# Kernel optimization log

Measured on AMD Instinct MI355X. Metric: run time of the kernel, lower is better.

## Reference

```python
import jax, jax.numpy as jnp
import numpy as np

H, DI, N, R, B, L, K = 1024, 2048, 16, 64, 1, 2048, 4


def setup_inputs() -> dict:
    key = jax.random.key(0)
    ks = jax.random.split(key, 12)
    s = 0.02
    x = jax.random.normal(ks[0], (B, L, H), dtype=jnp.float32)
    in_proj_w = jax.random.normal(ks[1], (2 * DI, H), dtype=jnp.float32) * s
    in_proj_b = jax.random.normal(ks[2], (2 * DI,), dtype=jnp.float32) * s
    conv_w = jax.random.normal(ks[3], (DI, 1, K), dtype=jnp.float32) * s
    conv_b = jax.random.normal(ks[4], (DI,), dtype=jnp.float32) * s
    x_proj_w = jax.random.normal(ks[5], (R + 2 * N, DI), dtype=jnp.float32) * s
    dt_init_std = R ** (-0.5)
    dt_proj_w = jax.random.uniform(ks[6], (DI, R), dtype=jnp.float32, minval=-dt_init_std, maxval=dt_init_std)
    dt = jnp.exp(jax.random.uniform(ks[7], (DI,), dtype=jnp.float32) * (np.log(0.1) - np.log(0.001)) + np.log(0.001))
    dt = jnp.clip(dt, 0.0001, None)
    dt_proj_b = dt + jnp.log(-jnp.expm1(-dt))
    A_log = jnp.log(jnp.broadcast_to(jnp.arange(1, N + 1, dtype=jnp.float32)[None, :], (DI, N)))
    D = jnp.ones((DI,), dtype=jnp.float32)
    out_proj_w = jax.random.normal(ks[8], (H, DI), dtype=jnp.float32) * s
    return {"x": x, "in_proj_w": in_proj_w, "in_proj_b": in_proj_b, "conv_w": conv_w,
            "conv_b": conv_b, "x_proj_w": x_proj_w, "dt_proj_w": dt_proj_w,
            "dt_proj_b": dt_proj_b, "A_log": A_log, "D": D, "out_proj_w": out_proj_w}


def _mamba_fwd(x, in_proj_w, in_proj_b, conv_w, conv_b, x_proj_w, dt_proj_w, dt_proj_b, A_log, D, out_proj_w):
    b, l, _ = x.shape
    x_and_res = x @ in_proj_w.T + in_proj_b               # [b, l, 2*DI]
    xc, res = jnp.split(x_and_res, 2, axis=-1)
    # causal depthwise conv1d (padding K-1 then truncate to l == left-pad only)
    xt = jnp.transpose(xc, (0, 2, 1))                     # [b, DI, l]
    conv = jax.lax.conv_general_dilated(
        xt, conv_w, window_strides=(1,), padding=[(K - 1, 0)],
        dimension_numbers=("NCH", "OIH", "NCH"), feature_group_count=DI)
    conv = conv + conv_b[None, :, None]
    xs = jnp.transpose(jax.nn.silu(conv), (0, 2, 1))      # [b, l, DI]
    # SSM
    A = -jnp.exp(A_log.astype(jnp.float32))               # [DI, N]
    x_dbl = xs @ x_proj_w.T                               # [b, l, R+2N]
    delta, Bm, Cm = jnp.split(x_dbl, [R, R + N], axis=-1)
    delta = jax.nn.softplus(delta @ dt_proj_w.T + dt_proj_b)   # [b, l, DI]
    deltaA = jnp.exp(delta[..., None] * A[None, None])         # [b, l, DI, N]
    deltaB_u = delta[..., None] * Bm[:, :, None, :] * xs[..., None]

    def comb(c1, c2):
        a1, u1 = c1
        a2, u2 = c2
        return a2 * a1, a2 * u1 + u2

    _, h = jax.lax.associative_scan(comb, (deltaA, deltaB_u), axis=1)
    y = jnp.einsum("bldn,bln->bld", h, Cm) + xs * D.astype(jnp.float32)
    y = y * jax.nn.silu(res)
    return y @ out_proj_w.T                               # [b, l, H]


def reference(x, in_proj_w, in_proj_b, conv_w, conv_b, x_proj_w, dt_proj_w, dt_proj_b, A_log, D, out_proj_w):
    return _mamba_fwd(x, in_proj_w, in_proj_b, conv_w, conv_b, x_proj_w,
                      dt_proj_w, dt_proj_b, A_log, D, out_proj_w)
```

## Files before the change

kernel.cpp:

```cpp
#include <hip/hip_runtime.h>
#include <hip/hip_bf16.h>
#include <math.h>

#define H_DIM 1024
#define DI    2048
#define NS    16
#define RR    64
#define LL    2048
#define NC    32
#define CL    64
#define KSPL  16

typedef __bf16 bf16x8 __attribute__((ext_vector_type(8)));
typedef __bf16 bf16x4 __attribute__((ext_vector_type(4)));
typedef float  f32x4  __attribute__((ext_vector_type(4)));

__device__ __forceinline__ float silu_f(float x)  { return x / (1.f + __expf(-x)); }
__device__ __forceinline__ float softplus_f(float x) {
    const float l = __logf(1.f + __expf(x));
    return x > 15.f ? x : l;
}

__device__ __forceinline__ void gload16(const void* g, void* l) {
    __builtin_amdgcn_global_load_lds(
        (const __attribute__((address_space(1))) void*)g,
        (__attribute__((address_space(3))) void*)l, 16, 0, 0);
}

__device__ __forceinline__ void f2b4(const float* __restrict__ in,
                                     __bf16* __restrict__ out)
{
    float4 v = *(const float4*)in;
    bf16x4 o;
    o[0] = (__bf16)v.x; o[1] = (__bf16)v.y; o[2] = (__bf16)v.z; o[3] = (__bf16)v.w;
    *(bf16x4*)out = o;
}

#define SEG0 (LL * H_DIM)
#define SEG1 (2 * DI * H_DIM)
#define SEG2 (H_DIM * DI)
#define SEG3 (DI * RR)
#define SEG4 (128 * DI)
#define CUM0 SEG0
#define CUM1 (CUM0 + SEG1)
#define CUM2 (CUM1 + SEG2)
#define CUM3 (CUM2 + SEG3)
#define CUMT (CUM3 + SEG4)

__global__ __launch_bounds__(256) void convert_all_k(
    const float* __restrict__ x,    const float* __restrict__ in_w,
    const float* __restrict__ outw, const float* __restrict__ dtw,
    const float* __restrict__ xpw,
    __bf16* __restrict__ x_bf,    __bf16* __restrict__ inw_bf,
    __bf16* __restrict__ outw_bf, __bf16* __restrict__ dtw_bf,
    __bf16* __restrict__ xpw_pad)
{
    const int i = (blockIdx.x * 256 + threadIdx.x) * 4;
    if (i < CUM0) {
        f2b4(x + i, x_bf + i);
    } else if (i < CUM1) {
        const int o = i - CUM0;  f2b4(in_w + o, inw_bf + o);
    } else if (i < CUM2) {
        const int o = i - CUM1;  f2b4(outw + o, outw_bf + o);
    } else if (i < CUM3) {
        const int o = i - CUM2;  f2b4(dtw + o, dtw_bf + o);
    } else if (i < CUMT) {
        const int o = i - CUM3;
        const int row = o >> 11;
        if (row < 96) {
            f2b4(xpw + o, xpw_pad + o);
        } else {
            bf16x4 z; z[0] = z[1] = z[2] = z[3] = (__bf16)0.f;
            *(bf16x4*)&xpw_pad[o] = z;
        }
    }
}

__global__ __launch_bounds__(256) void reduce_xdbl_k(
    const float* __restrict__ part, float* __restrict__ xdbl,
    __bf16* __restrict__ xdbl_bf)
{
    const int idx = blockIdx.x * 256 + threadIdx.x;
    float s = 0.f;
    #pragma unroll
    for (int z = 0; z < KSPL; ++z) s += part[(size_t)z * (LL * 96) + idx];
    xdbl[idx] = s;
    xdbl_bf[idx] = (__bf16)s;
}

__global__ __launch_bounds__(256) void gemm_inproj_k(
    const __bf16* __restrict__ A,
    const __bf16* __restrict__ W,
    const float* __restrict__ bias,
    __bf16* __restrict__ xc_bf,
    __bf16* __restrict__ res_bf)
{
    __shared__ __bf16 smA[128 * 32];
    __shared__ __bf16 smB[128 * 32];
    const int t    = threadIdx.x;
    const int lane = t & 63;
    const int m0 = blockIdx.y * 128, n0 = blockIdx.x * 128;
    const int wr = ((t >> 6) >> 1) * 64;
    const int wc = ((t >> 6) & 1) * 64;

    const int srow = t >> 2;
    const int skof = (t & 3) * 8;
    const int lds_base = (t >> 6) * 512;

    const int offA = (wr + (lane & 15)) * 32 + ((lane >> 4) * 8);
    const int offB = (wc + (lane & 15)) * 32 + ((lane >> 4) * 8);

    f32x4 acc[4][4] = {};

    for (int k0 = 0; k0 < H_DIM; k0 += 32) {
        gload16(A + (size_t)(m0 + srow)      * H_DIM + k0 + skof, &smA[lds_base]);
        gload16(A + (size_t)(m0 + 64 + srow) * H_DIM + k0 + skof, &smA[2048 + lds_base]);
        gload16(W + (size_t)(n0 + srow)      * H_DIM + k0 + skof, &smB[lds_base]);
        gload16(W + (size_t)(n0 + 64 + srow) * H_DIM + k0 + skof, &smB[2048 + lds_base]);
        __syncthreads();

        bf16x8 af[4], bfr[4];
        #pragma unroll
        for (int m = 0; m < 4; ++m) af[m]  = *(const bf16x8*)&smA[offA + m * 512];
        #pragma unroll
        for (int n = 0; n < 4; ++n) bfr[n] = *(const bf16x8*)&smB[offB + n * 512];
        #pragma unroll
        for (int m = 0; m < 4; ++m)
            #pragma unroll
            for (int n = 0; n < 4; ++n)
                acc[m][n] = __builtin_amdgcn_mfma_f32_16x16x32_bf16(
                    af[m], bfr[n], acc[m][n], 0, 0, 0);
        __syncthreads();
    }

    __bf16* outp = (n0 < DI) ? xc_bf : res_bf;
    const int ncol0 = (n0 < DI) ? n0 : n0 - DI;
    const int rbase = m0 + wr + ((lane >> 4) << 2);
    const int cbase = ncol0 + wc + (lane & 15);
    #pragma unroll
    for (int n = 0; n < 4; ++n) {
        const int col = cbase + n * 16;
        const float bv = bias[(n0 < DI ? 0 : DI) + col];
        #pragma unroll
        for (int m = 0; m < 4; ++m)
            #pragma unroll
            for (int j = 0; j < 4; ++j)
                outp[(size_t)(rbase + m * 16 + j) * DI + col] =
                    (__bf16)(acc[m][n][j] + bv);
    }
}

template<int BIAS, int ACT, int SPLITK>
__global__ __launch_bounds__(256) void gemm64_bf16_nt(
    const __bf16* __restrict__ A, int lda,
    const __bf16* __restrict__ W, int ldw,
    const float* __restrict__ bias,
    float* __restrict__ C, int ldc, int ncols, size_t pstride,
    int K)
{
    __shared__ __bf16 smA[64 * 32];
    __shared__ __bf16 smB[128 * 32];
    const int t    = threadIdx.x;
    const int lane = t & 63;
    const int m0 = blockIdx.y * 64, n0 = blockIdx.x * 128;
    const int wr = ((t >> 6) >> 1) * 32;
    const int wc = ((t >> 6) & 1) * 64;

    const int srow = t >> 2;
    const int skof = (t & 3) * 8;
    const int lds_base = (t >> 6) * 512;

    const int offA = (wr + (lane & 15)) * 32 + ((lane >> 4) * 8);
    const int offB = (wc + (lane & 15)) * 32 + ((lane >> 4) * 8);

    const int kseg  = K / SPLITK;
    const int kbase = (SPLITK > 1) ? blockIdx.z * kseg : 0;

    f32x4 acc[2][4] = {};

    for (int k0 = kbase; k0 < kbase + kseg; k0 += 32) {
        gload16(A + (size_t)(m0 + srow)      * lda + k0 + skof, &smA[lds_base]);
        gload16(W + (size_t)(n0 + srow)      * ldw + k0 + skof, &smB[lds_base]);
        gload16(W + (size_t)(n0 + 64 + srow) * ldw + k0 + skof, &smB[2048 + lds_base]);
        __syncthreads();

        bf16x8 af[2], bfr[4];
        #pragma unroll
        for (int m = 0; m < 2; ++m) af[m]  = *(const bf16x8*)&smA[offA + m * 512];
        #pragma unroll
        for (int n = 0; n < 4; ++n) bfr[n] = *(const bf16x8*)&smB[offB + n * 512];
        #pragma unroll
        for (int m = 0; m < 2; ++m)
            #pragma unroll
            for (int n = 0; n < 4; ++n)
                acc[m][n] = __builtin_amdgcn_mfma_f32_16x16x32_bf16(
                    af[m], bfr[n], acc[m][n], 0, 0, 0);
        __syncthreads();
    }

    float* Cp = C + ((SPLITK > 1) ? (size_t)blockIdx.z * pstride : 0);
    const int rbase = m0 + wr + ((lane >> 4) << 2);
    const int cbase = n0 + wc + (lane & 15);
    #pragma unroll
    for (int n = 0; n < 4; ++n) {
        const int col = cbase + n * 16;
        if (col >= ncols) continue;
        const float bv = BIAS ? bias[col] : 0.f;
        #pragma unroll
        for (int m = 0; m < 2; ++m) {
            #pragma unroll
            for (int j = 0; j < 4; ++j) {
                float v = acc[m][n][j] + bv;
                if (ACT == 1) v = softplus_f(v);
                Cp[(size_t)(rbase + m * 16 + j) * ldc + col] = v;
            }
        }
    }
}

__global__ __launch_bounds__(256) void conv_silu_k(
    const __bf16* __restrict__ xc, const float* __restrict__ cw,
    const float* __restrict__ cb, __bf16* __restrict__ xs_bf)
{
    const int idx = blockIdx.x * 256 + threadIdx.x;
    const int l  = idx >> 8;
    const int d0 = (idx & 255) * 8;

    float r0[8] = {}, r1[8] = {}, r2[8] = {}, r3[8];
    bf16x8 v;
    if (l >= 3) { v = *(const bf16x8*)&xc[(size_t)(l-3)*DI + d0];
                  #pragma unroll
                  for (int j = 0; j < 8; ++j) r0[j] = (float)v[j]; }
    if (l >= 2) { v = *(const bf16x8*)&xc[(size_t)(l-2)*DI + d0];
                  #pragma unroll
                  for (int j = 0; j < 8; ++j) r1[j] = (float)v[j]; }
    if (l >= 1) { v = *(const bf16x8*)&xc[(size_t)(l-1)*DI + d0];
                  #pragma unroll
                  for (int j = 0; j < 8; ++j) r2[j] = (float)v[j]; }
    v = *(const bf16x8*)&xc[(size_t)l*DI + d0];
    #pragma unroll
    for (int j = 0; j < 8; ++j) r3[j] = (float)v[j];

    bf16x8 o;
    #pragma unroll
    for (int j = 0; j < 8; ++j) {
        const int d = d0 + j;
        float4 w = *(const float4*)&cw[d * 4];
        float a = cb[d];
        a = fmaf(r0[j], w.x, a);
        a = fmaf(r1[j], w.y, a);
        a = fmaf(r2[j], w.z, a);
        a = fmaf(r3[j], w.w, a);
        o[j] = (__bf16)silu_f(a);
    }
    *(bf16x8*)&xs_bf[(size_t)l*DI + d0] = o;
}

__global__ __launch_bounds__(256) void scan1_k(
    const float* __restrict__ delta, const __bf16* __restrict__ xs,
    const float* __restrict__ A_log, const float* __restrict__ xdbl,
    float* __restrict__ P, float* __restrict__ S)
{
    const int d = blockIdx.x * 256 + threadIdx.x;
    const int c = blockIdx.y;
    float A[NS];
    #pragma unroll
    for (int n = 0; n < NS; ++n) A[n] = -__expf(A_log[d * NS + n]);
    float h[NS] = {};
    float ap[NS];
    #pragma unroll
    for (int n = 0; n < NS; ++n) ap[n] = 1.f;

    const int l0 = c * CL;
    for (int l = l0; l < l0 + CL; ++l) {
        const float dt = delta[(size_t)l * DI + d];
        const float u  = (float)xs[(size_t)l * DI + d];
        const float du = dt * u;
        #pragma unroll
        for (int n = 0; n < NS; ++n) {
            const float Bn = xdbl[(size_t)l * 96 + RR + n];
            const float dA = __expf(dt * A[n]);
            h[n]  = fmaf(dA, h[n], du * Bn);
            ap[n] *= dA;
        }
    }
    const size_t base = ((size_t)c * DI + d) * NS;
    #pragma unroll
    for (int n = 0; n < NS; ++n) { P[base + n] = ap[n]; S[base + n] = h[n]; }
}

__global__ __launch_bounds__(256) void scan2_k(
    const float* __restrict__ P, const float* __restrict__ S, float* __restrict__ Hp)
{
    const int idx = blockIdx.x * 256 + threadIdx.x;
    float h = 0.f;
    for (int c = 0; c < NC; ++c) {
        const size_t o = (size_t)c * DI * NS + idx;
        Hp[o] = h;
        h = fmaf(P[o], h, S[o]);
    }
}

__global__ __launch_bounds__(256) void scan3_k(
    const float* __restrict__ delta, const __bf16* __restrict__ xs,
    const float* __restrict__ A_log, const float* __restrict__ xdbl,
    const float* __restrict__ Hp, const __bf16* __restrict__ res_bf,
    const float* __restrict__ Dp, __bf16* __restrict__ y_bf)
{
    const int d = blockIdx.x * 256 + threadIdx.x;
    const int c = blockIdx.y;
    float A[NS];
    #pragma unroll
    for (int n = 0; n < NS; ++n) A[n] = -__expf(A_log[d * NS + n]);
    float h[NS];
    const size_t base = ((size_t)c * DI + d) * NS;
    #pragma unroll
    for (int n = 0; n < NS; ++n) h[n] = Hp[base + n];
    const float Dd = Dp[d];

    const int l0 = c * CL;
    for (int l = l0; l < l0 + CL; ++l) {
        const float dt = delta[(size_t)l * DI + d];
        const float u  = (float)xs[(size_t)l * DI + d];
        const float du = dt * u;
        float acc = 0.f;
        #pragma unroll
        for (int n = 0; n < NS; ++n) {
            const float Bn = xdbl[(size_t)l * 96 + RR + n];
            const float Cn = xdbl[(size_t)l * 96 + RR + NS + n];
            const float dA = __expf(dt * A[n]);
            h[n] = fmaf(dA, h[n], du * Bn);
            acc  = fmaf(h[n], Cn, acc);
        }
        float yv = fmaf(u, Dd, acc);
        const float r = (float)res_bf[(size_t)l * DI + d];
        yv *= silu_f(r);
        y_bf[(size_t)l * DI + d] = (__bf16)yv;
    }
}

extern "C" void kernel_launch(void* const* d_in, const int* in_sizes, int n_in,
                              void* d_out, int out_size, void* d_ws, size_t ws_size,
                              hipStream_t stream)
{
    const float* x        = (const float*)d_in[0];
    const float* in_w     = (const float*)d_in[1];
    const float* in_b     = (const float*)d_in[2];
    const float* conv_w   = (const float*)d_in[3];
    const float* conv_b   = (const float*)d_in[4];
    const float* xproj_w  = (const float*)d_in[5];
    const float* dtproj_w = (const float*)d_in[6];
    const float* dtproj_b = (const float*)d_in[7];
    const float* A_log    = (const float*)d_in[8];
    const float* Dp       = (const float*)d_in[9];
    const float* outw     = (const float*)d_in[10];
    float* out = (float*)d_out;

    float* ws    = (float*)d_ws;
    float* delta = ws;
    float* xdbl  = delta + (size_t)LL * DI;
    float* P     = xdbl  + (size_t)LL * 96;
    float* S     = P     + (size_t)NC * DI * NS;
    float* Hp    = S     + (size_t)NC * DI * NS;
    float* xpart = delta;
    __bf16* x_bf    = (__bf16*)(Hp + (size_t)NC * DI * NS);
    __bf16* inw_bf  = x_bf    + (size_t)LL * H_DIM;
    __bf16* outw_bf = inw_bf  + (size_t)2 * DI * H_DIM;
    __bf16* dtw_bf  = outw_bf + (size_t)H_DIM * DI;
    __bf16* xdbl_bf = dtw_bf  + (size_t)DI * RR;
    __bf16* y_bf    = xdbl_bf + (size_t)LL * 96;
    __bf16* xs_bf   = y_bf    + (size_t)LL * DI;
    __bf16* xc_bf   = xs_bf   + (size_t)LL * DI;
    __bf16* res_bf  = xc_bf   + (size_t)LL * DI;
    __bf16* xpw_pad = res_bf  + (size_t)LL * DI;

    const dim3 blk(256);

    convert_all_k<<<dim3(CUMT / 1024), blk, 0, stream>>>(
        x, in_w, outw, dtproj_w, xproj_w,
        x_bf, inw_bf, outw_bf, dtw_bf, xpw_pad);

    gemm_inproj_k<<<dim3((2*DI)/128, LL/128), blk, 0, stream>>>(
        x_bf, inw_bf, in_b, xc_bf, res_bf);

    conv_silu_k<<<dim3((LL*DI)/(8*256)), blk, 0, stream>>>(xc_bf, conv_w, conv_b, xs_bf);

    gemm64_bf16_nt<0,0,KSPL><<<dim3(1, LL/64, KSPL), blk, 0, stream>>>(
        xs_bf, DI, xpw_pad, DI, nullptr, xpart, 96, 96, (size_t)LL * 96, DI);
    reduce_xdbl_k<<<dim3((LL * 96) / 256), blk, 0, stream>>>(xpart, xdbl, xdbl_bf);

    gemm64_bf16_nt<1,1,1><<<dim3(DI/128, LL/64), blk, 0, stream>>>(
        xdbl_bf, 96, dtw_bf, RR, dtproj_b, delta, DI, DI, 0, RR);

    scan1_k<<<dim3(DI/256, NC), blk, 0, stream>>>(delta, xs_bf, A_log, xdbl, P, S);
    scan2_k<<<dim3((DI*NS)/256), blk, 0, stream>>>(P, S, Hp);
    scan3_k<<<dim3(DI/256, NC), blk, 0, stream>>>(delta, xs_bf, A_log, xdbl, Hp, res_bf, Dp, y_bf);

    gemm64_bf16_nt<0,0,1><<<dim3(H_DIM/128, LL/64), blk, 0, stream>>>(
        y_bf, DI, outw_bf, DI, nullptr, out, H_DIM, H_DIM, 0, DI);
}
```

Measured before the change: 269.0 us.

## Double-buffer LDS tiles in GEMMs and add XCD-aware block swizzle

Converts the in-projection and generic bf16 GEMM kernels to double-buffered LDS staging, so the next K-tile's global-to-LDS loads are issued before the MFMAs on the current tile, with one barrier per iteration instead of two. It also adds a workgroup-index swizzle that maps consecutive tiles onto the same XCD, aiming for better L2 reuse; this is applied to the in-projection, dt-projection and out-projection GEMMs. The cost is doubled LDS use, which may reduce occupancy. The global_load_lds writes are not explicitly waited on before the barrier, so correctness depends on the compiler inserting vmcnt waits at __syncthreads.

Measured after the change: 268.1 us. Within noise of the previous version (-0.3%).

```diff
diff --git a/kernel.cpp b/kernel.cpp
--- a/kernel.cpp
+++ b/kernel.cpp
@@ -34,6 +34,15 @@
     bf16x4 o;
     o[0] = (__bf16)v.x; o[1] = (__bf16)v.y; o[2] = (__bf16)v.z; o[3] = (__bf16)v.w;
     *(bf16x4*)out = o;
+}
+
+__device__ __forceinline__ void xcd_swz(int nx, int ny, int& bx, int& by)
+{
+    const int nwg = nx * ny;
+    const int bid = by * nx + bx;
+    const int cpx = nwg >> 3;
+    const int s   = (bid & 7) * cpx + (bid >> 3);
+    bx = s % nx;  by = s / nx;
 }
 
 #define SEG0 (LL * H_DIM)
@@ -95,11 +104,13 @@
     __bf16* __restrict__ xc_bf,
     __bf16* __restrict__ res_bf)
 {
-    __shared__ __bf16 smA[128 * 32];
-    __shared__ __bf16 smB[128 * 32];
+    __shared__ __bf16 smA[2][128 * 32];
+    __shared__ __bf16 smB[2][128 * 32];
     const int t    = threadIdx.x;
     const int lane = t & 63;
-    const int m0 = blockIdx.y * 128, n0 = blockIdx.x * 128;
+    int bx = blockIdx.x, by = blockIdx.y;
+    xcd_swz(32, 16, bx, by);
+    const int m0 = by * 128, n0 = bx * 128;
     const int wr = ((t >> 6) >> 1) * 64;
     const int wc = ((t >> 6) & 1) * 64;
 
@@ -112,18 +123,25 @@
 
     f32x4 acc[4][4] = {};
 
+#define STAGE_IP(buf, k0)                                                          \
+    do {                                                                           \
+        gload16(A + (size_t)(m0 + srow)      * H_DIM + (k0) + skof, &smA[buf][lds_base]);        \
+        gload16(A + (size_t)(m0 + 64 + srow) * H_DIM + (k0) + skof, &smA[buf][2048 + lds_base]); \
+        gload16(W + (size_t)(n0 + srow)      * H_DIM + (k0) + skof, &smB[buf][lds_base]);        \
+        gload16(W + (size_t)(n0 + 64 + srow) * H_DIM + (k0) + skof, &smB[buf][2048 + lds_base]); \
+    } while (0)
+
+    STAGE_IP(0, 0);
+    __syncthreads();
+    int cur = 0;
     for (int k0 = 0; k0 < H_DIM; k0 += 32) {
-        gload16(A + (size_t)(m0 + srow)      * H_DIM + k0 + skof, &smA[lds_base]);
-        gload16(A + (size_t)(m0 + 64 + srow) * H_DIM + k0 + skof, &smA[2048 + lds_base]);
-        gload16(W + (size_t)(n0 + srow)      * H_DIM + k0 + skof, &smB[lds_base]);
-        gload16(W + (size_t)(n0 + 64 + srow) * H_DIM + k0 + skof, &smB[2048 + lds_base]);
-        __syncthreads();
+        if (k0 + 32 < H_DIM) STAGE_IP(cur ^ 1, k0 + 32);
 
         bf16x8 af[4], bfr[4];
         #pragma unroll
-        for (int m = 0; m < 4; ++m) af[m]  = *(const bf16x8*)&smA[offA + m * 512];
-        #pragma unroll
-        for (int n = 0; n < 4; ++n) bfr[n] = *(const bf16x8*)&smB[offB + n * 512];
+        for (int m = 0; m < 4; ++m) af[m]  = *(const bf16x8*)&smA[cur][offA + m * 512];
+        #pragma unroll
+        for (int n = 0; n < 4; ++n) bfr[n] = *(const bf16x8*)&smB[cur][offB + n * 512];
         #pragma unroll
         for (int m = 0; m < 4; ++m)
             #pragma unroll
@@ -131,7 +149,9 @@
                 acc[m][n] = __builtin_amdgcn_mfma_f32_16x16x32_bf16(
                     af[m], bfr[n], acc[m][n], 0, 0, 0);
         __syncthreads();
-    }
+        cur ^= 1;
+    }
+#undef STAGE_IP
 
     __bf16* outp = (n0 < DI) ? xc_bf : res_bf;
     const int ncol0 = (n0 < DI) ? n0 : n0 - DI;
@@ -150,7 +170,7 @@
     }
 }
 
-template<int BIAS, int ACT, int SPLITK>
+template<int BIAS, int ACT, int SPLITK, int SWZ>
 __global__ __launch_bounds__(256) void gemm64_bf16_nt(
     const __bf16* __restrict__ A, int lda,
     const __bf16* __restrict__ W, int ldw,
@@ -158,11 +178,13 @@
     float* __restrict__ C, int ldc, int ncols, size_t pstride,
     int K)
 {
-    __shared__ __bf16 smA[64 * 32];
-    __shared__ __bf16 smB[128 * 32];
+    __shared__ __bf16 smA[2][64 * 32];
+    __shared__ __bf16 smB[2][128 * 32];
     const int t    = threadIdx.x;
     const int lane = t & 63;
-    const int m0 = blockIdx.y * 64, n0 = blockIdx.x * 128;
+    int bx = blockIdx.x, by = blockIdx.y;
+    if (SWZ) xcd_swz(gridDim.x, gridDim.y, bx, by);
+    const int m0 = by * 64, n0 = bx * 128;
     const int wr = ((t >> 6) >> 1) * 32;
     const int wc = ((t >> 6) & 1) * 64;
 
@@ -175,20 +197,28 @@
 
     const int kseg  = K / SPLITK;
     const int kbase = (SPLITK > 1) ? blockIdx.z * kseg : 0;
+    const int kend  = kbase + kseg;
 
     f32x4 acc[2][4] = {};
 
-    for (int k0 = kbase; k0 < kbase + kseg; k0 += 32) {
-        gload16(A + (size_t)(m0 + srow)      * lda + k0 + skof, &smA[lds_base]);
-        gload16(W + (size_t)(n0 + srow)      * ldw + k0 + skof, &smB[lds_base]);
-        gload16(W + (size_t)(n0 + 64 + srow) * ldw + k0 + skof, &smB[2048 + lds_base]);
-        __syncthreads();
+#define STAGE_64(buf, k0)                                                          \
+    do {                                                                           \
+        gload16(A + (size_t)(m0 + srow)      * lda + (k0) + skof, &smA[buf][lds_base]);        \
+        gload16(W + (size_t)(n0 + srow)      * ldw + (k0) + skof, &smB[buf][lds_base]);        \
+        gload16(W + (size_t)(n0 + 64 + srow) * ldw + (k0) + skof, &smB[buf][2048 + lds_base]); \
+    } while (0)
+
+    STAGE_64(0, kbase);
+    __syncthreads();
+    int cur = 0;
+    for (int k0 = kbase; k0 < kend; k0 += 32) {
+        if (k0 + 32 < kend) STAGE_64(cur ^ 1, k0 + 32);
 
         bf16x8 af[2], bfr[4];
         #pragma unroll
-        for (int m = 0; m < 2; ++m) af[m]  = *(const bf16x8*)&smA[offA + m * 512];
-        #pragma unroll
-        for (int n = 0; n < 4; ++n) bfr[n] = *(const bf16x8*)&smB[offB + n * 512];
+        for (int m = 0; m < 2; ++m) af[m]  = *(const bf16x8*)&smA[cur][offA + m * 512];
+        #pragma unroll
+        for (int n = 0; n < 4; ++n) bfr[n] = *(const bf16x8*)&smB[cur][offB + n * 512];
         #pragma unroll
         for (int m = 0; m < 2; ++m)
             #pragma unroll
@@ -196,7 +226,9 @@
                 acc[m][n] = __builtin_amdgcn_mfma_f32_16x16x32_bf16(
                     af[m], bfr[n], acc[m][n], 0, 0, 0);
         __syncthreads();
-    }
+        cur ^= 1;
+    }
+#undef STAGE_64
 
     float* Cp = C + ((SPLITK > 1) ? (size_t)blockIdx.z * pstride : 0);
     const int rbase = m0 + wr + ((lane >> 4) << 2);
@@ -385,17 +417,17 @@
 
     conv_silu_k<<<dim3((LL*DI)/(8*256)), blk, 0, stream>>>(xc_bf, conv_w, conv_b, xs_bf);
 
-    gemm64_bf16_nt<0,0,KSPL><<<dim3(1, LL/64, KSPL), blk, 0, stream>>>(
+    gemm64_bf16_nt<0,0,KSPL,0><<<dim3(1, LL/64, KSPL), blk, 0, stream>>>(
         xs_bf, DI, xpw_pad, DI, nullptr, xpart, 96, 96, (size_t)LL * 96, DI);
     reduce_xdbl_k<<<dim3((LL * 96) / 256), blk, 0, stream>>>(xpart, xdbl, xdbl_bf);
 
-    gemm64_bf16_nt<1,1,1><<<dim3(DI/128, LL/64), blk, 0, stream>>>(
+    gemm64_bf16_nt<1,1,1,1><<<dim3(DI/128, LL/64), blk, 0, stream>>>(
         xdbl_bf, 96, dtw_bf, RR, dtproj_b, delta, DI, DI, 0, RR);
 
     scan1_k<<<dim3(DI/256, NC), blk, 0, stream>>>(delta, xs_bf, A_log, xdbl, P, S);
     scan2_k<<<dim3((DI*NS)/256), blk, 0, stream>>>(P, S, Hp);
     scan3_k<<<dim3(DI/256, NC), blk, 0, stream>>>(delta, xs_bf, A_log, xdbl, Hp, res_bf, Dp, y_bf);
 
-    gemm64_bf16_nt<0,0,1><<<dim3(H_DIM/128, LL/64), blk, 0, stream>>>(
+    gemm64_bf16_nt<0,0,1,1><<<dim3(H_DIM/128, LL/64), blk, 0, stream>>>(
         y_bf, DI, outw_bf, DI, nullptr, out, H_DIM, H_DIM, 0, DI);
 }
```
